# Kernel tuning notes

Measured on AMD Instinct MI355X. Metric: run time of the kernel, lower is better.

## Reference

```python
import jax, jax.numpy as jnp
import numpy as np

WH, WW = 7, 7
N = WH * WW
HEADS = 12
HEAD_DIM = 16
EMBED = 384
INNER = HEADS * HEAD_DIM
NW = 64
B_ = 2048
SCALE = HEAD_DIM ** -0.5


def _relative_position_index():
    ch, cw = np.meshgrid(np.arange(WH), np.arange(WW), indexing='ij')
    coords = np.stack([ch.ravel(), cw.ravel()])              # [2, N]
    rel = coords[:, :, None] - coords[:, None, :]             # [2, N, N]
    rel = rel.transpose(1, 2, 0)
    rel[:, :, 0] += WH - 1
    rel[:, :, 1] += WW - 1
    rel[:, :, 0] *= 2 * WW - 1
    return jnp.asarray(rel.sum(-1), dtype=jnp.int32)          # [N, N]


def setup_inputs() -> dict:
    key = jax.random.key(0)
    ks = jax.random.split(key, 8)
    s_in = EMBED ** -0.5
    s_inner = INNER ** -0.5
    x = jax.random.normal(ks[0], (B_, N, EMBED), jnp.float32)
    # Swin shift mask: 0 or -100 per window pair
    mbits = jax.random.bernoulli(ks[1], 0.2, (NW, N, N))
    mask = jnp.where(mbits, jnp.float32(-100.0), jnp.float32(0.0))
    return {
        'x': x,
        'mask': mask,
        'Wq': jax.random.normal(ks[2], (EMBED, INNER), jnp.float32) * s_in,
        'bq': jnp.zeros((INNER,), jnp.float32),
        'Wk': jax.random.normal(ks[3], (EMBED, INNER), jnp.float32) * s_in,
        'bk': jnp.zeros((INNER,), jnp.float32),
        'Wv': jax.random.normal(ks[4], (EMBED, INNER), jnp.float32) * s_in,
        'bv': jnp.zeros((INNER,), jnp.float32),
        'Wp': jax.random.normal(ks[5], (INNER, EMBED), jnp.float32) * s_inner,
        'bp': jnp.zeros((EMBED,), jnp.float32),
        'bias_table': jax.random.normal(ks[6], ((2 * WH - 1) * (2 * WW - 1), HEADS), jnp.float32) * 0.02,
        'rel_idx': _relative_position_index(),
    }


def reference(x, mask, Wq, bq, Wk, bk, Wv, bv, Wp, bp, bias_table, rel_idx):
    B, n, _ = x.shape
    q = (x @ Wq + bq).reshape(B, n, HEADS, HEAD_DIM)
    k = (x @ Wk + bk).reshape(B, n, HEADS, HEAD_DIM)
    v = (x @ Wv + bv).reshape(B, n, HEADS, HEAD_DIM)
    attn = jnp.einsum('bnhd,bmhd->bhnm', q * SCALE, k)        # [B, H, N, N]
    bias = bias_table[rel_idx]                                 # [N, N, H]
    attn = attn + jnp.transpose(bias, (2, 0, 1))[None]
    nW = mask.shape[0]
    attn = attn.reshape(B // nW, nW, HEADS, n, n) + mask[None, :, None]
    attn = jax.nn.softmax(attn.reshape(B, HEADS, n, n), axis=-1)
    out = jnp.einsum('bhnm,bmhd->bnhd', attn, v).reshape(B, n, INNER)
    return out @ Wp + bp
```

## Files before the change

kernel.cpp:

```cpp
#include <hip/hip_runtime.h>


typedef __attribute__((ext_vector_type(8))) short  bf8;
typedef __attribute__((ext_vector_type(4))) short  bf4;
typedef __attribute__((ext_vector_type(4))) float  f4;

union B8 { bf8 v; unsigned u[4]; };

__device__ __forceinline__ short f2b(float f) {
  unsigned u = __builtin_bit_cast(unsigned, f);
  unsigned r = u + 0x7fffu + ((u >> 16) & 1u);
  return (short)(r >> 16);
}
__device__ __forceinline__ unsigned pk2(float lo, float hi) {
  return (unsigned)(unsigned short)f2b(lo) | ((unsigned)(unsigned short)f2b(hi) << 16);
}
__device__ __forceinline__ unsigned dperm(int addr, unsigned lo, unsigned hi, bool glo) {
  int a = __builtin_amdgcn_ds_bpermute(addr, (int)lo);
  int b = __builtin_amdgcn_ds_bpermute(addr, (int)hi);
  return (unsigned)(glo ? a : b);
}

__global__ void wa_prep(const float* __restrict__ Wq, const float* __restrict__ Wk,
                        const float* __restrict__ Wv, const float* __restrict__ Wp,
                        const float* __restrict__ btab, const int* __restrict__ ridx,
                        short* __restrict__ wt, short* __restrict__ wpt,
                        float* __restrict__ biasCT) {
  int id = blockIdx.x * 256 + threadIdx.x;
  const int NWT = 576 * 384, NWP = 384 * 192, NBC = 12 * 64 * 64;
  if (id < NWT) {
    int row = id / 384, k = id - row * 384;
    int kind = row / 192, cc = row - kind * 192;
    const float* W = (kind == 0) ? Wq : (kind == 1 ? Wk : Wv);
    float v = W[k * 192 + cc];
    if (kind == 0) v *= 0.25f;
    wt[id] = f2b(v);
  } else if ((id -= NWT) < NWP) {
    int n = id / 192, k = id - n * 192;
    wpt[id] = f2b(Wp[k * 384 + n]);
  } else if ((id -= NWP) < NBC) {
    int h = id / 4096, rem = id - h * 4096;
    int n = rem >> 6, m = rem & 63;
    biasCT[id] = (m < 49 && n < 49) ? btab[ridx[m * 49 + n] * 12 + h] : 0.f;
  }
}

struct __align__(16) Smem {
  union U {
    short xs[64][392];
    struct QK { short qs[64][200]; short ks[64][200]; } qk;
  } u;
  float maskT[64][68];
};

__global__ __launch_bounds__(256, 2)
void wa_main(const float* __restrict__ x, const float* __restrict__ mask,
             const float* __restrict__ bq, const float* __restrict__ bk,
             const float* __restrict__ bv, const float* __restrict__ bp,
             const short* __restrict__ wt, const short* __restrict__ wpt,
             const float* __restrict__ biasCT, float* __restrict__ out) {
  __shared__ Smem sm;
  const int tid = threadIdx.x;
  const int w   = tid >> 6;
  const int lid = tid & 63;
  const int g   = lid >> 4;
  const int c   = lid & 15;
  const int blk = blockIdx.x;

  {
    const float* xw = x + (size_t)blk * 18816;
    f4 xv[18];
#pragma unroll
    for (int it = 0; it < 18; it++) {
      int i = tid + it * 256;
      xv[it] = *(const f4*)(xw + (i / 96) * 384 + (i % 96) * 4);
    }
    const int iT = tid + 18 * 256;
    f4 xt = {0.f, 0.f, 0.f, 0.f};
    if (iT < 4704) xt = *(const f4*)(xw + (iT / 96) * 384 + (iT % 96) * 4);
    const float* mw = mask + (size_t)(blk & 63) * 2401;
    float mv[17];
#pragma unroll
    for (int it = 0; it < 17; it++) {
      int i = tid + it * 256;
      int n = i / 68, m = i - n * 68;
      mv[it] = (n < 49 && m < 49) ? mw[m * 49 + n] : 0.f;
    }
#pragma unroll
    for (int it = 0; it < 18; it++) {
      int i = tid + it * 256;
      bf4 pk = {f2b(xv[it][0]), f2b(xv[it][1]), f2b(xv[it][2]), f2b(xv[it][3])};
      *(bf4*)&sm.u.xs[i / 96][(i % 96) * 4] = pk;
    }
    if (iT < 4704) {
      bf4 pk = {f2b(xt[0]), f2b(xt[1]), f2b(xt[2]), f2b(xt[3])};
      *(bf4*)&sm.u.xs[iT / 96][(iT % 96) * 4] = pk;
    }
    const bf8 zz = {0,0,0,0,0,0,0,0};
#pragma unroll
    for (int it = 0; it < 3; it++) {
      int i = tid + it * 256;
      if (i < 735) { int row = 49 + i / 49, c8 = (i % 49) * 8; *(bf8*)&sm.u.xs[row][c8] = zz; }
    }
#pragma unroll
    for (int it = 0; it < 17; it++) {
      int i = tid + it * 256;
      sm.maskT[i / 68][i % 68] = mv[it];
    }
  }
  __syncthreads();

  f4 acc[4][9];
#pragma unroll
  for (int mt = 0; mt < 4; mt++)
#pragma unroll
    for (int i = 0; i < 9; i++) acc[mt][i] = (f4){0.f, 0.f, 0.f, 0.f};
  int rowb[9];
#pragma unroll
  for (int i = 0; i < 9; i++) {
    int kind = i / 3, hh = 3 * w + i % 3;
    rowb[i] = (kind * 192 + hh * 16 + c) * 384;
  }
#pragma unroll 3
  for (int ks = 0; ks < 12; ks++) {
    const int k0 = ks * 32 + g * 8;
    bf8 a[4], b[9];
#pragma unroll
    for (int mt = 0; mt < 4; mt++) a[mt] = *(const bf8*)&sm.u.xs[mt * 16 + c][k0];
#pragma unroll
    for (int i = 0; i < 9; i++) b[i] = *(const bf8*)(wt + rowb[i] + k0);
#pragma unroll
    for (int mt = 0; mt < 4; mt++)
#pragma unroll
      for (int i = 0; i < 9; i++)
        acc[mt][i] = __builtin_amdgcn_mfma_f32_16x16x32_bf16(a[mt], b[i], acc[mt][i], 0, 0, 0);
  }
  __syncthreads();

  unsigned vpk[3][4][2];
#pragma unroll
  for (int i = 0; i < 9; i++) {
    const int kind = i / 3, hh = 3 * w + i % 3;
    const int col = hh * 16 + c;
    const float bb = (kind == 0) ? 0.25f * bq[col] : (kind == 1 ? bk[col] : bv[col]);
#pragma unroll
    for (int mt = 0; mt < 4; mt++) {
      if (kind == 2) {
        vpk[i - 6][mt][0] = pk2(acc[mt][i][0] + bb, acc[mt][i][1] + bb);
        vpk[i - 6][mt][1] = pk2(acc[mt][i][2] + bb, acc[mt][i][3] + bb);
      } else {
        short* dst = (kind == 0) ? &sm.u.qk.qs[0][0] : &sm.u.qk.ks[0][0];
#pragma unroll
        for (int r = 0; r < 4; r++)
          dst[(mt * 16 + g * 4 + r) * 200 + col] = f2b(acc[mt][i][r] + bb);
      }
    }
  }
  asm volatile("" ::: "memory");

  const int  addrA = c * 4 + (((2 * g)     & 3) << 6);
  const int  addrB = c * 4 + (((2 * g + 1) & 3) << 6);
  const bool glo   = (g < 2);
  const f4   z4 = {0.f, 0.f, 0.f, 0.f};
  const bf8  z8 = {0,0,0,0,0,0,0,0};
#pragma unroll
  for (int t = 0; t < 3; t++) {
    const int h  = 3 * w + t;
    const int hb = h * 16;
    bf8 afr[4], bfr[4];
#pragma unroll
    for (int nt = 0; nt < 4; nt++)
      afr[nt] = glo ? *(const bf8*)&sm.u.qk.ks[nt * 16 + c][hb + g * 8] : z8;
#pragma unroll
    for (int mt = 0; mt < 4; mt++)
      bfr[mt] = glo ? *(const bf8*)&sm.u.qk.qs[mt * 16 + c][hb + g * 8] : z8;
    f4 s[4][4];
#pragma unroll
    for (int nt = 0; nt < 4; nt++)
#pragma unroll
      for (int mt = 0; mt < 4; mt++)
        s[nt][mt] = __builtin_amdgcn_mfma_f32_16x16x32_bf16(afr[nt], bfr[mt], z4, 0, 0, 0);
#pragma unroll
    for (int nt = 0; nt < 4; nt++)
#pragma unroll
      for (int r = 0; r < 4; r++) {
        const int n = nt * 16 + g * 4 + r;
#pragma unroll
        for (int mt = 0; mt < 4; mt++) {
          const int m = mt * 16 + c;
          float v = s[nt][mt][r] + biasCT[(h * 64 + n) * 64 + m] + sm.maskT[n][m];
          s[nt][mt][r] = (n < 49) ? v : -1e30f;
        }
      }
#pragma unroll
    for (int mt = 0; mt < 4; mt++) {
      float mx = -3e38f;
#pragma unroll
      for (int nt = 0; nt < 4; nt++)
#pragma unroll
        for (int r = 0; r < 4; r++) mx = fmaxf(mx, s[nt][mt][r]);
      mx = fmaxf(mx, __shfl_xor(mx, 16, 64));
      mx = fmaxf(mx, __shfl_xor(mx, 32, 64));
      float sum = 0.f;
#pragma unroll
      for (int nt = 0; nt < 4; nt++)
#pragma unroll
        for (int r = 0; r < 4; r++) {
          float p = __expf(s[nt][mt][r] - mx);
          s[nt][mt][r] = p;
          sum += p;
        }
      sum += __shfl_xor(sum, 16, 64);
      sum += __shfl_xor(sum, 32, 64);
      const float rinv = 1.f / sum;
#pragma unroll
      for (int nt = 0; nt < 4; nt++)
#pragma unroll
        for (int r = 0; r < 4; r++) s[nt][mt][r] *= rinv;
    }
    unsigned ppk[4][4][2];
#pragma unroll
    for (int nt = 0; nt < 4; nt++)
#pragma unroll
      for (int mt = 0; mt < 4; mt++) {
        ppk[nt][mt][0] = pk2(s[nt][mt][0], s[nt][mt][1]);
        ppk[nt][mt][1] = pk2(s[nt][mt][2], s[nt][mt][3]);
      }
    f4 o[4];
#pragma unroll
    for (int mt = 0; mt < 4; mt++) o[mt] = z4;
#pragma unroll
    for (int ks2 = 0; ks2 < 2; ks2++) {
      B8 va;
      va.u[0] = dperm(addrA, vpk[t][2 * ks2][0], vpk[t][2 * ks2 + 1][0], glo);
      va.u[1] = dperm(addrA, vpk[t][2 * ks2][1], vpk[t][2 * ks2 + 1][1], glo);
      va.u[2] = dperm(addrB, vpk[t][2 * ks2][0], vpk[t][2 * ks2 + 1][0], glo);
      va.u[3] = dperm(addrB, vpk[t][2 * ks2][1], vpk[t][2 * ks2 + 1][1], glo);
#pragma unroll
      for (int mt = 0; mt < 4; mt++) {
        B8 pb;
        pb.u[0] = dperm(addrA, ppk[2 * ks2][mt][0], ppk[2 * ks2 + 1][mt][0], glo);
        pb.u[1] = dperm(addrA, ppk[2 * ks2][mt][1], ppk[2 * ks2 + 1][mt][1], glo);
        pb.u[2] = dperm(addrB, ppk[2 * ks2][mt][0], ppk[2 * ks2 + 1][mt][0], glo);
        pb.u[3] = dperm(addrB, ppk[2 * ks2][mt][1], ppk[2 * ks2 + 1][mt][1], glo);
        o[mt] = __builtin_amdgcn_mfma_f32_16x16x32_bf16(va.v, pb.v, o[mt], 0, 0, 0);
      }
    }
#pragma unroll
    for (int mt = 0; mt < 4; mt++) {
      bf4 pk = {f2b(o[mt][0]), f2b(o[mt][1]), f2b(o[mt][2]), f2b(o[mt][3])};
      *(bf4*)&sm.u.qk.qs[mt * 16 + c][hb + g * 4] = pk;
    }
    asm volatile("" ::: "memory");
  }
  __syncthreads();

  f4 acc3[6][4];
#pragma unroll
  for (int jt = 0; jt < 6; jt++)
#pragma unroll
    for (int mt = 0; mt < 4; mt++) acc3[jt][mt] = z4;
#pragma unroll 2
  for (int ks3 = 0; ks3 < 6; ks3++) {
    const int k0 = ks3 * 32 + g * 8;
    bf8 ao[4], wb[6];
#pragma unroll
    for (int mt = 0; mt < 4; mt++) ao[mt] = *(const bf8*)&sm.u.qk.qs[mt * 16 + c][k0];
#pragma unroll
    for (int jt = 0; jt < 6; jt++)
      wb[jt] = *(const bf8*)(wpt + (w * 96 + jt * 16 + c) * 192 + k0);
#pragma unroll
    for (int jt = 0; jt < 6; jt++)
#pragma unroll
      for (int mt = 0; mt < 4; mt++)
        acc3[jt][mt] = __builtin_amdgcn_mfma_f32_16x16x32_bf16(wb[jt], ao[mt], acc3[jt][mt], 0, 0, 0);
  }
  float* ow = out + (size_t)blk * 18816;
#pragma unroll
  for (int jt = 0; jt < 6; jt++) {
    const int colb = w * 96 + jt * 16 + g * 4;
    const f4 bp4 = *(const f4*)&bp[colb];
#pragma unroll
    for (int mt = 0; mt < 4; mt++) {
      const int m = mt * 16 + c;
      if (m < 49) {
        f4 v = acc3[jt][mt] + bp4;
        *(f4*)&ow[m * 384 + colb] = v;
      }
    }
  }
}

extern "C" void kernel_launch(void* const* d_in, const int* in_sizes, int n_in,
                              void* d_out, int out_size, void* d_ws, size_t ws_size,
                              hipStream_t stream) {
  const float* x    = (const float*)d_in[0];
  const float* mask = (const float*)d_in[1];
  const float* Wq   = (const float*)d_in[2];
  const float* bq   = (const float*)d_in[3];
  const float* Wk   = (const float*)d_in[4];
  const float* bk   = (const float*)d_in[5];
  const float* Wv   = (const float*)d_in[6];
  const float* bv   = (const float*)d_in[7];
  const float* Wp   = (const float*)d_in[8];
  const float* bp   = (const float*)d_in[9];
  const float* btab = (const float*)d_in[10];
  const int*   ridx = (const int*)d_in[11];
  float* out = (float*)d_out;

  char* ws = (char*)d_ws;
  short* wt     = (short*)ws;
  short* wpt    = (short*)(ws + 442368);
  float* biasCT = (float*)(ws + 589824);

  wa_prep<<<dim3(1344), dim3(256), 0, stream>>>(Wq, Wk, Wv, Wp, btab, ridx, wt, wpt, biasCT);
  wa_main<<<dim3(2048), dim3(256), 0, stream>>>(x, mask, bq, bk, bv, bp, wt, wpt, biasCT, out);
}
```

Measured before the change: 269.0 us.

## Stage x in halves to shrink LDS, build K fragments via bpermute, raise occupancy

Shared memory shrinks to a single 64x200 bf16 buffer plus the mask by staging x into LDS in two 192-column halves. The QK projection and the V projection each run over both halves, so x is reloaded from global memory three times in total. The K fragments for QK^T are now assembled from registers with ds_bpermute instead of being read back from LDS, which removes the separate K buffer. Launch bounds go from 2 to 3 blocks per SM to use the freed LDS, at the cost of extra global x traffic, more barriers and register pressure.

```diff
diff --git a/kernel.cpp b/kernel.cpp
--- a/kernel.cpp
+++ b/kernel.cpp
@@ -46,14 +46,31 @@
 }
 
 struct __align__(16) Smem {
-  union U {
-    short xs[64][392];
-    struct QK { short qs[64][200]; short ks[64][200]; } qk;
-  } u;
+  short qs[64][200];
   float maskT[64][68];
 };
 
-__global__ __launch_bounds__(256, 2)
+#define STAGE_HALF(HOFF)                                                     \
+  {                                                                          \
+    f4 xv[10];                                                               \
+    _Pragma("unroll")                                                        \
+    for (int it = 0; it < 10; it++) {                                        \
+      int i = tid + it * 256;                                                \
+      int row = i / 48, c4 = (i - row * 48) * 4;                             \
+      if (i < 2352) xv[it] = *(const f4*)(xw + row * 384 + (HOFF) + c4);     \
+    }                                                                        \
+    _Pragma("unroll")                                                        \
+    for (int it = 0; it < 10; it++) {                                        \
+      int i = tid + it * 256;                                                \
+      int row = i / 48, c4 = (i - row * 48) * 4;                             \
+      if (i < 2352) {                                                        \
+        bf4 pk = {f2b(xv[it][0]), f2b(xv[it][1]), f2b(xv[it][2]), f2b(xv[it][3])}; \
+        *(bf4*)&sm.qs[row][c4] = pk;                                         \
+      }                                                                      \
+    }                                                                        \
+  }
+
+__global__ __launch_bounds__(256, 3)
 void wa_main(const float* __restrict__ x, const float* __restrict__ mask,
              const float* __restrict__ bq, const float* __restrict__ bk,
              const float* __restrict__ bv, const float* __restrict__ bp,
@@ -66,18 +83,15 @@
   const int g   = lid >> 4;
   const int c   = lid & 15;
   const int blk = blockIdx.x;
+  const float* xw = x + (size_t)blk * 18816;
 
   {
-    const float* xw = x + (size_t)blk * 18816;
-    f4 xv[18];
-#pragma unroll
-    for (int it = 0; it < 18; it++) {
+    const bf8 zz = {0,0,0,0,0,0,0,0};
+#pragma unroll
+    for (int it = 0; it < 2; it++) {
       int i = tid + it * 256;
-      xv[it] = *(const f4*)(xw + (i / 96) * 384 + (i % 96) * 4);
-    }
-    const int iT = tid + 18 * 256;
-    f4 xt = {0.f, 0.f, 0.f, 0.f};
-    if (iT < 4704) xt = *(const f4*)(xw + (iT / 96) * 384 + (iT % 96) * 4);
+      if (i < 360) { int row = 49 + i / 24, c8 = (i % 24) * 8; *(bf8*)&sm.qs[row][c8] = zz; }
+    }
     const float* mw = mask + (size_t)(blk & 63) * 2401;
     float mv[17];
 #pragma unroll
@@ -87,93 +101,169 @@
       mv[it] = (n < 49 && m < 49) ? mw[m * 49 + n] : 0.f;
     }
 #pragma unroll
-    for (int it = 0; it < 18; it++) {
-      int i = tid + it * 256;
-      bf4 pk = {f2b(xv[it][0]), f2b(xv[it][1]), f2b(xv[it][2]), f2b(xv[it][3])};
-      *(bf4*)&sm.u.xs[i / 96][(i % 96) * 4] = pk;
-    }
-    if (iT < 4704) {
-      bf4 pk = {f2b(xt[0]), f2b(xt[1]), f2b(xt[2]), f2b(xt[3])};
-      *(bf4*)&sm.u.xs[iT / 96][(iT % 96) * 4] = pk;
-    }
-    const bf8 zz = {0,0,0,0,0,0,0,0};
-#pragma unroll
-    for (int it = 0; it < 3; it++) {
-      int i = tid + it * 256;
-      if (i < 735) { int row = 49 + i / 49, c8 = (i % 49) * 8; *(bf8*)&sm.u.xs[row][c8] = zz; }
-    }
-#pragma unroll
     for (int it = 0; it < 17; it++) {
       int i = tid + it * 256;
       sm.maskT[i / 68][i % 68] = mv[it];
     }
-  }
-  __syncthreads();
-
-  f4 acc[4][9];
+    STAGE_HALF(0)
+  }
+  __syncthreads();
+
+  f4 acc6[4][6];
 #pragma unroll
   for (int mt = 0; mt < 4; mt++)
 #pragma unroll
-    for (int i = 0; i < 9; i++) acc[mt][i] = (f4){0.f, 0.f, 0.f, 0.f};
-  int rowb[9];
-#pragma unroll
-  for (int i = 0; i < 9; i++) {
-    int kind = i / 3, hh = 3 * w + i % 3;
-    rowb[i] = (kind * 192 + hh * 16 + c) * 384;
-  }
-#pragma unroll 3
-  for (int ks = 0; ks < 12; ks++) {
+    for (int i = 0; i < 6; i++) acc6[mt][i] = (f4){0.f, 0.f, 0.f, 0.f};
+  int rqk[6];
+#pragma unroll
+  for (int i = 0; i < 6; i++) rqk[i] = ((i / 3) * 192 + (3 * w + i % 3) * 16 + c) * 384;
+
+#pragma unroll 2
+  for (int ks = 0; ks < 6; ks++) {
     const int k0 = ks * 32 + g * 8;
-    bf8 a[4], b[9];
-#pragma unroll
-    for (int mt = 0; mt < 4; mt++) a[mt] = *(const bf8*)&sm.u.xs[mt * 16 + c][k0];
-#pragma unroll
-    for (int i = 0; i < 9; i++) b[i] = *(const bf8*)(wt + rowb[i] + k0);
-#pragma unroll
-    for (int mt = 0; mt < 4; mt++)
-#pragma unroll
-      for (int i = 0; i < 9; i++)
-        acc[mt][i] = __builtin_amdgcn_mfma_f32_16x16x32_bf16(a[mt], b[i], acc[mt][i], 0, 0, 0);
-  }
-  __syncthreads();
-
+    bf8 a[4], b[6];
+#pragma unroll
+    for (int mt = 0; mt < 4; mt++) a[mt] = *(const bf8*)&sm.qs[mt * 16 + c][k0];
+#pragma unroll
+    for (int i = 0; i < 6; i++) b[i] = *(const bf8*)(wt + rqk[i] + k0);
+#pragma unroll
+    for (int mt = 0; mt < 4; mt++)
+#pragma unroll
+      for (int i = 0; i < 6; i++)
+        acc6[mt][i] = __builtin_amdgcn_mfma_f32_16x16x32_bf16(a[mt], b[i], acc6[mt][i], 0, 0, 0);
+  }
+  __syncthreads();
+  STAGE_HALF(192)
+  __syncthreads();
+#pragma unroll 2
+  for (int ks = 0; ks < 6; ks++) {
+    const int k0 = ks * 32 + g * 8;
+    bf8 a[4], b[6];
+#pragma unroll
+    for (int mt = 0; mt < 4; mt++) a[mt] = *(const bf8*)&sm.qs[mt * 16 + c][k0];
+#pragma unroll
+    for (int i = 0; i < 6; i++) b[i] = *(const bf8*)(wt + rqk[i] + 192 + k0);
+#pragma unroll
+    for (int mt = 0; mt < 4; mt++)
+#pragma unroll
+      for (int i = 0; i < 6; i++)
+        acc6[mt][i] = __builtin_amdgcn_mfma_f32_16x16x32_bf16(a[mt], b[i], acc6[mt][i], 0, 0, 0);
+  }
+  unsigned qpk[3][4][2], kpk[3][4][2];
+#pragma unroll
+  for (int i = 0; i < 3; i++) {
+    const int col = (3 * w + i) * 16 + c;
+    const float bqv = 0.25f * bq[col], bkv = bk[col];
+#pragma unroll
+    for (int mt = 0; mt < 4; mt++) {
+      qpk[i][mt][0] = pk2(acc6[mt][i][0] + bqv, acc6[mt][i][1] + bqv);
+      qpk[i][mt][1] = pk2(acc6[mt][i][2] + bqv, acc6[mt][i][3] + bqv);
+      kpk[i][mt][0] = pk2(acc6[mt][3 + i][0] + bkv, acc6[mt][3 + i][1] + bkv);
+      kpk[i][mt][1] = pk2(acc6[mt][3 + i][2] + bkv, acc6[mt][3 + i][3] + bkv);
+    }
+  }
+
+  f4 acc3[4][3];
+#pragma unroll
+  for (int mt = 0; mt < 4; mt++)
+#pragma unroll
+    for (int i = 0; i < 3; i++) acc3[mt][i] = (f4){0.f, 0.f, 0.f, 0.f};
+  int rv[3];
+#pragma unroll
+  for (int i = 0; i < 3; i++) rv[i] = (384 + (3 * w + i) * 16 + c) * 384;
+
+#pragma unroll 2
+  for (int ks = 0; ks < 6; ks++) {
+    const int k0 = ks * 32 + g * 8;
+    bf8 a[4], b[3];
+#pragma unroll
+    for (int mt = 0; mt < 4; mt++) a[mt] = *(const bf8*)&sm.qs[mt * 16 + c][k0];
+#pragma unroll
+    for (int i = 0; i < 3; i++) b[i] = *(const bf8*)(wt + rv[i] + 192 + k0);
+#pragma unroll
+    for (int mt = 0; mt < 4; mt++)
+#pragma unroll
+      for (int i = 0; i < 3; i++)
+        acc3[mt][i] = __builtin_amdgcn_mfma_f32_16x16x32_bf16(a[mt], b[i], acc3[mt][i], 0, 0, 0);
+  }
+  __syncthreads();
+  STAGE_HALF(0)
+  __syncthreads();
+#pragma unroll 2
+  for (int ks = 0; ks < 6; ks++) {
+    const int k0 = ks * 32 + g * 8;
+    bf8 a[4], b[3];
+#pragma unroll
+    for (int mt = 0; mt < 4; mt++) a[mt] = *(const bf8*)&sm.qs[mt * 16 + c][k0];
+#pragma unroll
+    for (int i = 0; i < 3; i++) b[i] = *(const bf8*)(wt + rv[i] + k0);
+#pragma unroll
+    for (int mt = 0; mt < 4; mt++)
+#pragma unroll
+      for (int i = 0; i < 3; i++)
+        acc3[mt][i] = __builtin_amdgcn_mfma_f32_16x16x32_bf16(a[mt], b[i], acc3[mt][i], 0, 0, 0);
+  }
   unsigned vpk[3][4][2];
 #pragma unroll
-  for (int i = 0; i < 9; i++) {
-    const int kind = i / 3, hh = 3 * w + i % 3;
-    const int col = hh * 16 + c;
-    const float bb = (kind == 0) ? 0.25f * bq[col] : (kind == 1 ? bk[col] : bv[col]);
+  for (int i = 0; i < 3; i++) {
+    const int col = (3 * w + i) * 16 + c;
+    const float bvv = bv[col];
 #pragma unroll
     for (int mt = 0; mt < 4; mt++) {
-      if (kind == 2) {
-        vpk[i - 6][mt][0] = pk2(acc[mt][i][0] + bb, acc[mt][i][1] + bb);
-        vpk[i - 6][mt][1] = pk2(acc[mt][i][2] + bb, acc[mt][i][3] + bb);
-      } else {
-        short* dst = (kind == 0) ? &sm.u.qk.qs[0][0] : &sm.u.qk.ks[0][0];
-#pragma unroll
-        for (int r = 0; r < 4; r++)
-          dst[(mt * 16 + g * 4 + r) * 200 + col] = f2b(acc[mt][i][r] + bb);
-      }
-    }
+      vpk[i][mt][0] = pk2(acc3[mt][i][0] + bvv, acc3[mt][i][1] + bvv);
+      vpk[i][mt][1] = pk2(acc3[mt][i][2] + bvv, acc3[mt][i][3] + bvv);
+    }
+  }
+  __syncthreads();
+
+#pragma unroll
+  for (int i = 0; i < 3; i++) {
+    const int col = (3 * w + i) * 16 + c;
+#pragma unroll
+    for (int mt = 0; mt < 4; mt++)
+#pragma unroll
+      for (int rp = 0; rp < 2; rp++) {
+        unsigned wv = qpk[i][mt][rp];
+        sm.qs[mt * 16 + g * 4 + 2 * rp][col]     = (short)(wv & 0xFFFFu);
+        sm.qs[mt * 16 + g * 4 + 2 * rp + 1][col] = (short)(wv >> 16);
+      }
   }
   asm volatile("" ::: "memory");
 
   const int  addrA = c * 4 + (((2 * g)     & 3) << 6);
   const int  addrB = c * 4 + (((2 * g + 1) & 3) << 6);
   const bool glo   = (g < 2);
+  const int  abase4 = ((c >> 2) * 16 + (g & 1) * 8) * 4;
+  const bool csel  = (c & 2) != 0;
+  const bool chal  = (c & 1) != 0;
   const f4   z4 = {0.f, 0.f, 0.f, 0.f};
   const bf8  z8 = {0,0,0,0,0,0,0,0};
 #pragma unroll
   for (int t = 0; t < 3; t++) {
     const int h  = 3 * w + t;
     const int hb = h * 16;
-    bf8 afr[4], bfr[4];
-#pragma unroll
-    for (int nt = 0; nt < 4; nt++)
-      afr[nt] = glo ? *(const bf8*)&sm.u.qk.ks[nt * 16 + c][hb + g * 8] : z8;
-#pragma unroll
-    for (int mt = 0; mt < 4; mt++)
-      bfr[mt] = glo ? *(const bf8*)&sm.u.qk.qs[mt * 16 + c][hb + g * 8] : z8;
+    bf8 afr[4];
+#pragma unroll
+    for (int nt = 0; nt < 4; nt++) {
+      B8 af;
+#pragma unroll
+      for (int ep = 0; ep < 4; ep++) {
+        int a0 = abase4 + ep * 8;
+        unsigned A0 = (unsigned)__builtin_amdgcn_ds_bpermute(a0,     (int)kpk[t][nt][0]);
+        unsigned A1 = (unsigned)__builtin_amdgcn_ds_bpermute(a0,     (int)kpk[t][nt][1]);
+        unsigned B0 = (unsigned)__builtin_amdgcn_ds_bpermute(a0 + 4, (int)kpk[t][nt][0]);
+        unsigned B1 = (unsigned)__builtin_amdgcn_ds_bpermute(a0 + 4, (int)kpk[t][nt][1]);
+        unsigned Wa = csel ? A1 : A0, Wb = csel ? B1 : B0;
+        unsigned lo = (Wa & 0xFFFFu) | (Wb << 16);
+        unsigned hi = (Wa >> 16)     | (Wb & 0xFFFF0000u);
+        af.u[ep] = chal ? hi : lo;
+      }
+      afr[nt] = glo ? af.v : z8;
+    }
+    bf8 bfr[4];
+#pragma unroll
+    for (int mt = 0; mt < 4; mt++)
+      bfr[mt] = glo ? *(const bf8*)&sm.qs[mt * 16 + c][hb + g * 8] : z8;
     f4 s[4][4];
 #pragma unroll
     for (int nt = 0; nt < 4; nt++)
@@ -249,23 +339,23 @@
 #pragma unroll
     for (int mt = 0; mt < 4; mt++) {
       bf4 pk = {f2b(o[mt][0]), f2b(o[mt][1]), f2b(o[mt][2]), f2b(o[mt][3])};
-      *(bf4*)&sm.u.qk.qs[mt * 16 + c][hb + g * 4] = pk;
+      *(bf4*)&sm.qs[mt * 16 + c][hb + g * 4] = pk;
     }
     asm volatile("" ::: "memory");
   }
   __syncthreads();
 
-  f4 acc3[6][4];
+  f4 acc9[6][4];
 #pragma unroll
   for (int jt = 0; jt < 6; jt++)
 #pragma unroll
-    for (int mt = 0; mt < 4; mt++) acc3[jt][mt] = z4;
+    for (int mt = 0; mt < 4; mt++) acc9[jt][mt] = z4;
 #pragma unroll 2
   for (int ks3 = 0; ks3 < 6; ks3++) {
     const int k0 = ks3 * 32 + g * 8;
     bf8 ao[4], wb[6];
 #pragma unroll
-    for (int mt = 0; mt < 4; mt++) ao[mt] = *(const bf8*)&sm.u.qk.qs[mt * 16 + c][k0];
+    for (int mt = 0; mt < 4; mt++) ao[mt] = *(const bf8*)&sm.qs[mt * 16 + c][k0];
 #pragma unroll
     for (int jt = 0; jt < 6; jt++)
       wb[jt] = *(const bf8*)(wpt + (w * 96 + jt * 16 + c) * 192 + k0);
@@ -273,7 +363,7 @@
     for (int jt = 0; jt < 6; jt++)
 #pragma unroll
       for (int mt = 0; mt < 4; mt++)
-        acc3[jt][mt] = __builtin_amdgcn_mfma_f32_16x16x32_bf16(wb[jt], ao[mt], acc3[jt][mt], 0, 0, 0);
+        acc9[jt][mt] = __builtin_amdgcn_mfma_f32_16x16x32_bf16(wb[jt], ao[mt], acc9[jt][mt], 0, 0, 0);
   }
   float* ow = out + (size_t)blk * 18816;
 #pragma unroll
@@ -284,7 +374,7 @@
     for (int mt = 0; mt < 4; mt++) {
       const int m = mt * 16 + c;
       if (m < 49) {
-        f4 v = acc3[jt][mt] + bp4;
+        f4 v = acc9[jt][mt] + bp4;
         *(f4*)&ow[m * 384 + colb] = v;
       }
     }
```

Result: slower. 357.6 us (+32.9%).
